# Kernel optimization log

Measured on AMD Instinct MI355X. Metric: run time of the kernel, lower is better.

The kernel has to match this reference:

```python
import jax, jax.numpy as jnp
import numpy as np

D_MODEL = 768
N_HEADS = 12
D_FF = 3072
EPS = 1e-5


def layer_norm(x, gamma, beta):
    mu = jnp.mean(x, axis=-1, keepdims=True)
    var = jnp.mean(jnp.square(x - mu), axis=-1, keepdims=True)
    return (x - mu) * jax.lax.rsqrt(var + EPS) * gamma + beta


def setup_inputs() -> dict:
    key = jax.random.key(0)
    ks = jax.random.split(key, 8)
    s = 1.0 / np.sqrt(D_MODEL)
    sf = 1.0 / np.sqrt(D_FF)
    return {
        "x": jax.random.normal(ks[0], (2, 2048, D_MODEL), dtype=jnp.float32),
        "w_qkv": jax.random.uniform(ks[1], (D_MODEL, 3 * D_MODEL), jnp.float32, -s, s),
        "b_qkv": jnp.zeros((3 * D_MODEL,), jnp.float32),
        "w_out": jax.random.uniform(ks[2], (D_MODEL, D_MODEL), jnp.float32, -s, s),
        "b_out": jnp.zeros((D_MODEL,), jnp.float32),
        "w1": jax.random.uniform(ks[3], (D_MODEL, D_FF), jnp.float32, -s, s),
        "b1": jnp.zeros((D_FF,), jnp.float32),
        "w2": jax.random.uniform(ks[4], (D_FF, D_MODEL), jnp.float32, -sf, sf),
        "b2": jnp.zeros((D_MODEL,), jnp.float32),
        "g1": jnp.ones((D_MODEL,), jnp.float32),
        "be1": jnp.zeros((D_MODEL,), jnp.float32),
        "g2": jnp.ones((D_MODEL,), jnp.float32),
        "be2": jnp.zeros((D_MODEL,), jnp.float32),
    }


def reference(x, w_qkv, b_qkv, w_out, b_out, w1, b1, w2, b2, g1, be1, g2, be2):
    B, S, D = x.shape
    H = N_HEADS
    dk = D // H
    qkv = x @ w_qkv + b_qkv                      # [B,S,3D]
    q, k, v = jnp.split(qkv, 3, axis=-1)
    # [B,H,S,dk]
    q = q.reshape(B, S, H, dk).transpose(0, 2, 1, 3)
    k = k.reshape(B, S, H, dk).transpose(0, 2, 1, 3)
    v = v.reshape(B, S, H, dk).transpose(0, 2, 1, 3)
    scores = jnp.einsum('bhqd,bhkd->bhqk', q, k) / np.sqrt(dk)  # [B,H,S,S]
    attn = jax.nn.softmax(scores, axis=-1)
    o = jnp.einsum('bhqk,bhkd->bhqd', attn, v)
    o = o.transpose(0, 2, 1, 3).reshape(B, S, D)
    attn_out = o @ w_out + b_out
    x = layer_norm(x + attn_out, g1, be1)
    ffn = jax.nn.gelu(x @ w1 + b1, approximate=False) @ w2 + b2
    return layer_norm(x + ffn, g2, be2)
```

## Files before the change

kernel.cpp:

```cpp
#include <hip/hip_runtime.h>
#include <hip/hip_bf16.h>
#include <math.h>

#define D_MODEL 768
#define NH 12
#define DFF 3072
#define BB 2
#define SS 2048
#define MM (BB*SS)
#define DK 64

typedef _Float16 half8 __attribute__((ext_vector_type(8)));
typedef _Float16 half4 __attribute__((ext_vector_type(4)));
typedef float f32x4 __attribute__((ext_vector_type(4)));

template<int AM, int EPI>
__launch_bounds__(256)
__global__ void hgemm_k(const _Float16* __restrict__ A,
                        const _Float16* __restrict__ Bt,
                        const float* __restrict__ bias,
                        float* __restrict__ Cf, _Float16* __restrict__ Ch,
                        int M, int N, int K,
                        _Float16* __restrict__ qo, _Float16* __restrict__ ko,
                        _Float16* __restrict__ vo)
{
    constexpr int BM = AM * 32;
    constexpr int NA = BM / 8;
    __shared__ _Float16 Als[BM * 64];
    __shared__ _Float16 Bls[128 * 64];

    const int tid  = threadIdx.x;
    const int wv   = tid >> 6, lane = tid & 63;
    const int l15  = lane & 15, lg = lane >> 4;
    const int wr   = wv >> 1,  wc = wv & 1;
    const int m0   = blockIdx.y * BM, n0 = blockIdx.x * 128;

    f32x4 acc[AM][4];
    #pragma unroll
    for (int m = 0; m < AM; m++)
        #pragma unroll
        for (int n = 0; n < 4; n++)
            acc[m][n][0] = acc[m][n][1] = acc[m][n][2] = acc[m][n][3] = 0.0f;

    const char* Ab = (const char*)A;
    const char* Bb = (const char*)Bt;
    char* Al = (char*)Als;
    char* Bl = (char*)Bls;

    for (int kt = 0; kt < K; kt += 64) {
        __syncthreads();
        for (int inst = wv; inst < NA + 16; inst += 4) {
            const bool isA = inst < NA;
            const int  li  = isA ? inst : inst - NA;
            const int  p   = li * 1024 + lane * 16;
            const int  lo  = p ^ (((p >> 7) & 7) << 4);
            const int  row = lo >> 7, kb = lo & 127;
            const char* src = isA
                ? Ab + ((size_t)(m0 + row) * K + kt) * 2 + kb
                : Bb + ((size_t)(n0 + row) * K + kt) * 2 + kb;
            char* dst = (isA ? Al : Bl) + li * 1024;
            __builtin_amdgcn_global_load_lds(
                (const __attribute__((address_space(1))) void*)src,
                (__attribute__((address_space(3))) void*)dst, 16, 0, 0);
        }
        __syncthreads();

        #pragma unroll
        for (int ks = 0; ks < 2; ks++) {
            half8 af[AM], bf[4];
            #pragma unroll
            for (int m = 0; m < AM; m++) {
                int row = wr * (AM * 16) + m * 16 + l15;
                int off = (row * 128 + ks * 64 + lg * 16) ^ ((row & 7) << 4);
                af[m] = *(const half8*)(Al + off);
            }
            #pragma unroll
            for (int n = 0; n < 4; n++) {
                int row = wc * 64 + n * 16 + l15;
                int off = (row * 128 + ks * 64 + lg * 16) ^ ((row & 7) << 4);
                bf[n] = *(const half8*)(Bl + off);
            }
            #pragma unroll
            for (int m = 0; m < AM; m++)
                #pragma unroll
                for (int n = 0; n < 4; n++)
                    acc[m][n] = __builtin_amdgcn_mfma_f32_16x16x32_f16(
                        af[m], bf[n], acc[m][n], 0, 0, 0);
        }
    }

    #pragma unroll
    for (int m = 0; m < AM; m++) {
        #pragma unroll
        for (int n = 0; n < 4; n++) {
            int col = n0 + wc * 64 + n * 16 + l15;
            float bs = bias[col];
            #pragma unroll
            for (int r = 0; r < 4; r++) {
                int row = m0 + wr * (AM * 16) + m * 16 + lg * 4 + r;
                float val = acc[m][n][r] + bs;
                if (EPI == 0) {
                    Cf[(size_t)row * N + col] = val;
                } else if (EPI == 1) {
                    val = 0.5f * val * (1.0f + erff(val * 0.70710678118654752f));
                    Ch[(size_t)row * N + col] = (_Float16)val;
                } else {
                    int which = col / D_MODEL;
                    int c = col - which * D_MODEL;
                    int hh = c >> 6, dd = c & 63;
                    int bq = row >> 11, si = row & 2047;
                    _Float16 hv = (_Float16)val;
                    if (which == 0)
                        qo[((((size_t)bq * NH + hh) * SS) + si) * DK + dd] = hv;
                    else if (which == 1)
                        ko[((((size_t)bq * NH + hh) * SS) + si) * DK + dd] = hv;
                    else
                        vo[(((size_t)bq * NH + hh) * DK + dd) * SS + si] = hv;
                }
            }
        }
    }
}

__launch_bounds__(256)
__global__ void attn_mfma_k(const _Float16* __restrict__ Q,
                            const _Float16* __restrict__ K,
                            const _Float16* __restrict__ VT,
                            _Float16* __restrict__ O)
{
    __shared__ _Float16 Kls[2][64 * 64];
    __shared__ _Float16 Vls[2][64 * 64];
    __shared__ _Float16 Pl[4 * 1024];

    const int tid  = threadIdx.x;
    const int wv   = tid >> 6;
    const int lane = tid & 63;
    const int l15  = lane & 15;
    const int lg   = lane >> 4;

    const int bh = blockIdx.y;
    const int b  = bh / NH, h = bh - b * NH;
    const int q0 = blockIdx.x * 64 + wv * 16;

    const _Float16* Qb = Q + (size_t)bh * SS * DK;
    const char* Kb = (const char*)(K  + (size_t)bh * SS * DK);
    const char* Vb = (const char*)(VT + (size_t)bh * DK * SS);

#define ATTN_STAGE(buf, kt)                                                   \
    {                                                                         \
        _Pragma("unroll")                                                     \
        for (int w = 0; w < 4; w++) {                                         \
            int inst = wv + w * 4;                                            \
            bool isK = inst < 8;                                              \
            int li = isK ? inst : inst - 8;                                   \
            int p  = li * 1024 + lane * 16;                                   \
            int lo = p ^ (((p >> 7) & 7) << 4);                               \
            int row = lo >> 7, kbyte = lo & 127;                              \
            const char* src = isK                                             \
                ? (Kb + (size_t)((kt) + row) * 128 + kbyte)                   \
                : (Vb + (size_t)row * (SS * 2) + (size_t)(kt) * 2 + kbyte);   \
            char* dst = (isK ? (char*)Kls[buf] : (char*)Vls[buf]) + li * 1024;\
            __builtin_amdgcn_global_load_lds(                                 \
                (const __attribute__((address_space(1))) void*)src,           \
                (__attribute__((address_space(3))) void*)dst, 16, 0, 0);      \
        }                                                                     \
    }

    ATTN_STAGE(0, 0);

    half8 qa0 = *(const half8*)&Qb[(size_t)(q0 + l15) * DK + lg * 8];
    half8 qa1 = *(const half8*)&Qb[(size_t)(q0 + l15) * DK + 32 + lg * 8];
    #pragma unroll
    for (int i = 0; i < 8; i++) {
        qa0[i] = qa0[i] * (_Float16)0.125f;
        qa1[i] = qa1[i] * (_Float16)0.125f;
    }

    f32x4 po[4];
    float m_[4], l_[4];
    #pragma unroll
    for (int r = 0; r < 4; r++) {
        po[r][0] = po[r][1] = po[r][2] = po[r][3] = 0.0f;
        m_[r] = -1e30f; l_[r] = 0.0f;
    }

    char* Pw = (char*)&Pl[wv * 1024];
    const int prd = (l15 * 128 + lg * 16) ^ ((l15 & 7) << 4);

    asm volatile("s_waitcnt vmcnt(0)" ::: "memory");
    __syncthreads();

    for (int it = 0; it < SS / 64; ++it) {
        const int cur = it & 1;
        if (it + 1 < SS / 64) ATTN_STAGE(cur ^ 1, (it + 1) * 64);

        const char* Kc = (const char*)Kls[cur];
        const char* Vc = (const char*)Vls[cur];

        f32x4 sc[4];
        __builtin_amdgcn_s_setprio(1);
        #pragma unroll
        for (int t = 0; t < 4; t++) {
            int row = t * 16 + l15;
            int off0 = (row * 128 + lg * 16) ^ ((row & 7) << 4);
            int off1 = (row * 128 + 64 + lg * 16) ^ ((row & 7) << 4);
            half8 kb0 = *(const half8*)(Kc + off0);
            half8 kb1 = *(const half8*)(Kc + off1);
            f32x4 z;
            z[0] = z[1] = z[2] = z[3] = 0.0f;
            z = __builtin_amdgcn_mfma_f32_16x16x32_f16(qa0, kb0, z, 0, 0, 0);
            sc[t] = __builtin_amdgcn_mfma_f32_16x16x32_f16(qa1, kb1, z, 0, 0, 0);
        }
        __builtin_amdgcn_s_setprio(0);

        float rmv[4];
        float need = 0.0f;
        #pragma unroll
        for (int r = 0; r < 4; r++) {
            float rm = fmaxf(fmaxf(sc[0][r], sc[1][r]), fmaxf(sc[2][r], sc[3][r]));
            rm = fmaxf(rm, __shfl_xor(rm, 1));
            rm = fmaxf(rm, __shfl_xor(rm, 2));
            rm = fmaxf(rm, __shfl_xor(rm, 4));
            rm = fmaxf(rm, __shfl_xor(rm, 8));
            rmv[r] = rm;
            need = fmaxf(need, rm - m_[r]);
        }
        if (!__all(need <= 8.0f)) {
            #pragma unroll
            for (int r = 0; r < 4; r++) {
                float mn = fmaxf(m_[r], rmv[r]);
                float alpha = __expf(m_[r] - mn);
                m_[r] = mn;
                l_[r] *= alpha;
                #pragma unroll
                for (int dt = 0; dt < 4; dt++) po[dt][r] *= alpha;
            }
        }
        #pragma unroll
        for (int r = 0; r < 4; r++) {
            float rs = 0.0f;
            #pragma unroll
            for (int t = 0; t < 4; t++) {
                float p = __expf(sc[t][r] - m_[r]);
                sc[t][r] = p;
                rs += p;
            }
            rs += __shfl_xor(rs, 1);
            rs += __shfl_xor(rs, 2);
            rs += __shfl_xor(rs, 4);
            rs += __shfl_xor(rs, 8);
            l_[r] += rs;
        }

        #pragma unroll
        for (int t = 0; t < 4; t++)
            #pragma unroll
            for (int r = 0; r < 4; r++) {
                int row = lg * 4 + r, col = t * 16 + l15;
                int off = (row * 128 + col * 2) ^ ((row & 7) << 4);
                *(_Float16*)(Pw + off) = (_Float16)sc[t][r];
            }
        asm volatile("s_waitcnt lgkmcnt(0)" ::: "memory");
        __builtin_amdgcn_sched_barrier(0);

        half8 pa0 = *(const half8*)(Pw + prd);
        half8 pa1 = *(const half8*)(Pw + (prd ^ 64));

        __builtin_amdgcn_s_setprio(1);
        #pragma unroll
        for (int dt = 0; dt < 4; dt++) {
            int row = dt * 16 + l15;
            int off0 = (row * 128 + lg * 16) ^ ((row & 7) << 4);
            int off1 = (row * 128 + 64 + lg * 16) ^ ((row & 7) << 4);
            half8 vb0 = *(const half8*)(Vc + off0);
            half8 vb1 = *(const half8*)(Vc + off1);
            po[dt] = __builtin_amdgcn_mfma_f32_16x16x32_f16(pa0, vb0, po[dt], 0, 0, 0);
            po[dt] = __builtin_amdgcn_mfma_f32_16x16x32_f16(pa1, vb1, po[dt], 0, 0, 0);
        }
        __builtin_amdgcn_s_setprio(0);

        asm volatile("s_waitcnt vmcnt(0)" ::: "memory");
        __syncthreads();
    }
#undef ATTN_STAGE

    #pragma unroll
    for (int r = 0; r < 4; r++) {
        float inv = 1.0f / l_[r];
        int qrow = q0 + lg * 4 + r;
        size_t base = (size_t)(b * SS + qrow) * D_MODEL + h * DK;
        #pragma unroll
        for (int dt = 0; dt < 4; dt++)
            O[base + dt * 16 + l15] = (_Float16)(po[dt][r] * inv);
    }
}

template<bool RH, bool OH>
__launch_bounds__(256)
__global__ void ln_k(const void* __restrict__ xres, const float* __restrict__ y,
                     const float* __restrict__ gamma, const float* __restrict__ beta,
                     void* __restrict__ outp)
{
    const int row  = blockIdx.x * 4 + (threadIdx.x >> 6);
    const int lane = threadIdx.x & 63;
    const size_t base = (size_t)row * D_MODEL;

    float v[12];
    float sum = 0.0f, ssq = 0.0f;
    #pragma unroll
    for (int ch = 0; ch < 3; ch++) {
        int col = ch * 256 + lane * 4;
        float4 yv = *(const float4*)&y[base + col];
        float xr[4];
        if (RH) {
            half4 hv = *(const half4*)((const _Float16*)xres + base + col);
            #pragma unroll
            for (int i = 0; i < 4; i++) xr[i] = (float)hv[i];
        } else {
            float4 xv = *(const float4*)((const float*)xres + base + col);
            xr[0] = xv.x; xr[1] = xv.y; xr[2] = xv.z; xr[3] = xv.w;
        }
        float yy[4] = {yv.x, yv.y, yv.z, yv.w};
        #pragma unroll
        for (int i = 0; i < 4; i++) {
            float t = xr[i] + yy[i];
            v[ch * 4 + i] = t;
            sum += t;
            ssq += t * t;
        }
    }
    #pragma unroll
    for (int msk = 32; msk >= 1; msk >>= 1) {
        sum += __shfl_xor(sum, msk);
        ssq += __shfl_xor(ssq, msk);
    }

    const float mu  = sum * (1.0f / D_MODEL);
    const float var = ssq * (1.0f / D_MODEL) - mu * mu;
    const float inv = rsqrtf(var + 1e-5f);

    #pragma unroll
    for (int ch = 0; ch < 3; ch++) {
        int col = ch * 256 + lane * 4;
        float4 gv = *(const float4*)&gamma[col];
        float4 bv = *(const float4*)&beta[col];
        float g[4] = {gv.x, gv.y, gv.z, gv.w};
        float be[4] = {bv.x, bv.y, bv.z, bv.w};
        if (OH) {
            half4 o;
            #pragma unroll
            for (int i = 0; i < 4; i++)
                o[i] = (_Float16)((v[ch * 4 + i] - mu) * inv * g[i] + be[i]);
            *(half4*)((_Float16*)outp + base + col) = o;
        } else {
            float4 o;
            o.x = (v[ch * 4 + 0] - mu) * inv * g[0] + be[0];
            o.y = (v[ch * 4 + 1] - mu) * inv * g[1] + be[1];
            o.z = (v[ch * 4 + 2] - mu) * inv * g[2] + be[2];
            o.w = (v[ch * 4 + 3] - mu) * inv * g[3] + be[3];
            *(float4*)((float*)outp + base + col) = o;
        }
    }
}

__launch_bounds__(256)
__global__ void castx_k(const float* __restrict__ in, _Float16* __restrict__ out,
                        int n8)
{
    int i = blockIdx.x * 256 + threadIdx.x;
    if (i < n8) {
        float4 a = ((const float4*)in)[2 * i];
        float4 b = ((const float4*)in)[2 * i + 1];
        half8 h = {(_Float16)a.x, (_Float16)a.y, (_Float16)a.z, (_Float16)a.w,
                   (_Float16)b.x, (_Float16)b.y, (_Float16)b.z, (_Float16)b.w};
        ((half8*)out)[i] = h;
    }
}

__launch_bounds__(256)
__global__ void wcast_k(const float* __restrict__ src, _Float16* __restrict__ dst,
                        int K, int N)
{
    __shared__ float t[32][33];
    const int k0 = blockIdx.y * 32, n0 = blockIdx.x * 32;
    const int c = threadIdx.x & 31, r8 = threadIdx.x >> 5;
    #pragma unroll
    for (int rr = 0; rr < 4; rr++) {
        int r = rr * 8 + r8;
        t[r][c] = src[(size_t)(k0 + r) * N + n0 + c];
    }
    __syncthreads();
    #pragma unroll
    for (int rr = 0; rr < 4; rr++) {
        int n = rr * 8 + r8;
        dst[(size_t)(n0 + n) * K + k0 + c] = (_Float16)t[c][n];
    }
}

extern "C" void kernel_launch(void* const* d_in, const int* in_sizes, int n_in,
                              void* d_out, int out_size, void* d_ws, size_t ws_size,
                              hipStream_t stream)
{
    const float* x     = (const float*)d_in[0];
    const float* w_qkv = (const float*)d_in[1];
    const float* b_qkv = (const float*)d_in[2];
    const float* w_out = (const float*)d_in[3];
    const float* b_out = (const float*)d_in[4];
    const float* w1    = (const float*)d_in[5];
    const float* b1    = (const float*)d_in[6];
    const float* w2    = (const float*)d_in[7];
    const float* b2    = (const float*)d_in[8];
    const float* g1    = (const float*)d_in[9];
    const float* be1   = (const float*)d_in[10];
    const float* g2    = (const float*)d_in[11];
    const float* be2   = (const float*)d_in[12];

    char* w = (char*)d_ws;
    _Float16* q        = (_Float16*)(w);
    _Float16* kk       = (_Float16*)(w + 6291456);
    _Float16* vv       = (_Float16*)(w + 12582912);
    _Float16* ffn_h    = (_Float16*)(w);
    _Float16* xh       = (_Float16*)(w + 25165824);
    _Float16* attn_oh  = (_Float16*)(w + 25165824);
    _Float16* wqkvT    = (_Float16*)(w + 31457280);
    _Float16* woutT    = (_Float16*)(w + 34996224);
    _Float16* w1T      = (_Float16*)(w + 36175872);
    _Float16* w2T      = (_Float16*)(w + 40894464);
    float*    attn_proj= (float*)(w + 45613056);
    float*    ffn_out  = (float*)(w + 45613056);
    _Float16* x1h      = (_Float16*)(w + 58195968);
    float* out = (float*)d_out;

    dim3 blk(256);

    castx_k<<<(MM * D_MODEL / 8 + 255) / 256, blk, 0, stream>>>(x, xh, MM * D_MODEL / 8);
    wcast_k<<<dim3(2304 / 32, 768 / 32), blk, 0, stream>>>(w_qkv, wqkvT, 768, 2304);
    wcast_k<<<dim3(768 / 32, 768 / 32), blk, 0, stream>>>(w_out, woutT, 768, 768);
    wcast_k<<<dim3(3072 / 32, 768 / 32), blk, 0, stream>>>(w1, w1T, 768, 3072);
    wcast_k<<<dim3(768 / 32, 3072 / 32), blk, 0, stream>>>(w2, w2T, 3072, 768);

    hgemm_k<4, 2><<<dim3(2304 / 128, MM / 128), blk, 0, stream>>>(
        xh, wqkvT, b_qkv, nullptr, nullptr, MM, 2304, D_MODEL, q, kk, vv);

    attn_mfma_k<<<dim3(SS / 64, BB * NH), blk, 0, stream>>>(q, kk, vv, attn_oh);

    hgemm_k<2, 0><<<dim3(768 / 128, MM / 64), blk, 0, stream>>>(
        attn_oh, woutT, b_out, attn_proj, nullptr, MM, D_MODEL, D_MODEL,
        nullptr, nullptr, nullptr);

    ln_k<false, true><<<MM / 4, blk, 0, stream>>>(x, attn_proj, g1, be1, x1h);

    hgemm_k<4, 1><<<dim3(DFF / 128, MM / 128), blk, 0, stream>>>(
        x1h, w1T, b1, nullptr, ffn_h, MM, DFF, D_MODEL, nullptr, nullptr, nullptr);

    hgemm_k<2, 0><<<dim3(768 / 128, MM / 64), blk, 0, stream>>>(
        ffn_h, w2T, b2, ffn_out, nullptr, MM, D_MODEL, DFF, nullptr, nullptr, nullptr);

    ln_k<true, false><<<MM / 4, blk, 0, stream>>>(x1h, ffn_out, g2, be2, out);
}
```

Before: 344.8 us.

## Double-buffer GEMM LDS tiles and switch attention softmax to exp2 domain

```diff
diff --git a/kernel.cpp b/kernel.cpp
--- a/kernel.cpp
+++ b/kernel.cpp
@@ -26,8 +26,9 @@
 {
     constexpr int BM = AM * 32;
     constexpr int NA = BM / 8;
-    __shared__ _Float16 Als[BM * 64];
-    __shared__ _Float16 Bls[128 * 64];
+    constexpr int NI = NA + 16;
+    __shared__ _Float16 Als[2][BM * 64];
+    __shared__ _Float16 Bls[2][128 * 64];
 
     const int tid  = threadIdx.x;
     const int wv   = tid >> 6, lane = tid & 63;
@@ -44,27 +45,39 @@
 
     const char* Ab = (const char*)A;
     const char* Bb = (const char*)Bt;
-    char* Al = (char*)Als;
-    char* Bl = (char*)Bls;
-
-    for (int kt = 0; kt < K; kt += 64) {
-        __syncthreads();
-        for (int inst = wv; inst < NA + 16; inst += 4) {
-            const bool isA = inst < NA;
-            const int  li  = isA ? inst : inst - NA;
-            const int  p   = li * 1024 + lane * 16;
-            const int  lo  = p ^ (((p >> 7) & 7) << 4);
-            const int  row = lo >> 7, kb = lo & 127;
-            const char* src = isA
-                ? Ab + ((size_t)(m0 + row) * K + kt) * 2 + kb
-                : Bb + ((size_t)(n0 + row) * K + kt) * 2 + kb;
-            char* dst = (isA ? Al : Bl) + li * 1024;
-            __builtin_amdgcn_global_load_lds(
-                (const __attribute__((address_space(1))) void*)src,
-                (__attribute__((address_space(3))) void*)dst, 16, 0, 0);
-        }
-        __syncthreads();
-
+
+#define GSTAGE(buf, kt)                                                       \
+    {                                                                         \
+        _Pragma("unroll")                                                     \
+        for (int inst = wv; inst < NI; inst += 4) {                           \
+            const bool isA = inst < NA;                                       \
+            const int  li  = isA ? inst : inst - NA;                          \
+            const int  p   = li * 1024 + lane * 16;                           \
+            const int  lo  = p ^ (((p >> 7) & 7) << 4);                       \
+            const int  row = lo >> 7, kb = lo & 127;                          \
+            const char* src = isA                                             \
+                ? Ab + ((size_t)(m0 + row) * K + (kt)) * 2 + kb               \
+                : Bb + ((size_t)(n0 + row) * K + (kt)) * 2 + kb;              \
+            char* dst = (isA ? (char*)Als[buf] : (char*)Bls[buf]) + li * 1024;\
+            __builtin_amdgcn_global_load_lds(                                 \
+                (const __attribute__((address_space(1))) void*)src,           \
+                (__attribute__((address_space(3))) void*)dst, 16, 0, 0);      \
+        }                                                                     \
+    }
+
+    GSTAGE(0, 0);
+    asm volatile("s_waitcnt vmcnt(0)" ::: "memory");
+    __syncthreads();
+
+    const int nt = K >> 6;
+    for (int it = 0; it < nt; ++it) {
+        const int cur = it & 1;
+        if (it + 1 < nt) GSTAGE(cur ^ 1, (it + 1) << 6);
+
+        const char* Al = (const char*)Als[cur];
+        const char* Bl = (const char*)Bls[cur];
+
+        __builtin_amdgcn_s_setprio(1);
         #pragma unroll
         for (int ks = 0; ks < 2; ks++) {
             half8 af[AM], bf[4];
@@ -87,7 +100,12 @@
                     acc[m][n] = __builtin_amdgcn_mfma_f32_16x16x32_f16(
                         af[m], bf[n], acc[m][n], 0, 0, 0);
         }
-    }
+        __builtin_amdgcn_s_setprio(0);
+
+        asm volatile("s_waitcnt vmcnt(0)" ::: "memory");
+        __syncthreads();
+    }
+#undef GSTAGE
 
     #pragma unroll
     for (int m = 0; m < AM; m++) {
@@ -172,8 +190,8 @@
     half8 qa1 = *(const half8*)&Qb[(size_t)(q0 + l15) * DK + 32 + lg * 8];
     #pragma unroll
     for (int i = 0; i < 8; i++) {
-        qa0[i] = qa0[i] * (_Float16)0.125f;
-        qa1[i] = qa1[i] * (_Float16)0.125f;
+        qa0[i] = qa0[i] * (_Float16)0.18033688f;
+        qa1[i] = qa1[i] * (_Float16)0.18033688f;
     }
 
     f32x4 po[4];
@@ -225,11 +243,11 @@
             rmv[r] = rm;
             need = fmaxf(need, rm - m_[r]);
         }
-        if (!__all(need <= 8.0f)) {
+        if (!__all(need <= 11.5f)) {
             #pragma unroll
             for (int r = 0; r < 4; r++) {
                 float mn = fmaxf(m_[r], rmv[r]);
-                float alpha = __expf(m_[r] - mn);
+                float alpha = exp2f(m_[r] - mn);
                 m_[r] = mn;
                 l_[r] *= alpha;
                 #pragma unroll
@@ -241,7 +259,7 @@
             float rs = 0.0f;
             #pragma unroll
             for (int t = 0; t < 4; t++) {
-                float p = __expf(sc[t][r] - m_[r]);
+                float p = exp2f(sc[t][r] - m_[r]);
                 sc[t][r] = p;
                 rs += p;
             }
```

Measured after the change: 352.2 us. +2.1%, slower.
